# Optimization experiments

Hardware: AMD Instinct MI355X
Metric: run time of the kernel (lower is better)

The kernel has to match this reference:

```python
import jax, jax.numpy as jnp
import numpy as np

DIM = 768
NUM_HEADS = 12
HEAD_DIM = DIM // NUM_HEADS
SCALE = HEAD_DIM ** -0.5


def setup_inputs() -> dict:
    key = jax.random.key(0)
    k_x, k_qkv, k_proj, k_pb = jax.random.split(key, 4)
    B, N = 16, 1024
    x = jax.random.normal(k_x, (B, N, DIM), dtype=jnp.float32)
    # nn.Linear weights: stored as [out, in]; qkv_bias=False -> no qkv bias
    w_qkv = jax.random.normal(k_qkv, (3 * DIM, DIM), dtype=jnp.float32) * (DIM ** -0.5)
    w_proj = jax.random.normal(k_proj, (DIM, DIM), dtype=jnp.float32) * (DIM ** -0.5)
    b_proj = jax.random.normal(k_pb, (DIM,), dtype=jnp.float32) * 0.01
    return {"x": x, "w_qkv": w_qkv, "w_proj": w_proj, "b_proj": b_proj}


def reference(x, w_qkv, w_proj, b_proj):
    B, N, C = x.shape
    H, D = NUM_HEADS, HEAD_DIM
    # qkv projection: [B,N,3C] -> [3,B,H,N,D]
    qkv = jnp.einsum('bnc,oc->bno', x, w_qkv)
    qkv = qkv.reshape(B, N, 3, H, D).transpose(2, 0, 3, 1, 4)
    q, k, v = qkv[0], qkv[1], qkv[2]
    # scaled dot-product attention (dropout ratios are 0.0 -> identity)
    attn = jnp.einsum('bhnd,bhmd->bhnm', q, k) * SCALE
    attn = jax.nn.softmax(attn, axis=-1)
    out = jnp.einsum('bhnm,bhmd->bhnd', attn, v)
    out = out.transpose(0, 2, 1, 3).reshape(B, N, C)
    # output projection
    return jnp.einsum('bnc,oc->bno', out, w_proj) + b_proj
```

## Files before the change

### kernel.cpp

```cpp
#include <hip/hip_runtime.h>
#include <hip/hip_bf16.h>
#include <stdint.h>

typedef unsigned short u16;
typedef unsigned int   u32;
typedef short bf16x8 __attribute__((ext_vector_type(8)));
typedef float f32x4  __attribute__((ext_vector_type(4)));
typedef float f32x16 __attribute__((ext_vector_type(16)));

#define MFMA16(A,B,C) __builtin_amdgcn_mfma_f32_16x16x32_bf16((A),(B),(C),0,0,0)
#define MFMA32(A,B,C) __builtin_amdgcn_mfma_f32_32x32x16_bf16((A),(B),(C),0,0,0)

__device__ __forceinline__ u16 f2b(float x) {
  u32 u = __float_as_uint(x);
  u += 0x7fffu + ((u >> 16) & 1u);
  return (u16)(u >> 16);
}
__device__ __forceinline__ u32 cvtpk(float lo, float hi) {
  u32 r;
  asm("v_cvt_pk_bf16_f32 %0, %1, %2" : "=v"(r) : "v"(lo), "v"(hi));
  return r;
}

typedef __attribute__((address_space(1))) const void glob_void;
typedef __attribute__((address_space(3))) void lds_void;
__device__ __forceinline__ void gld16(const void* g, void* s) {
  __builtin_amdgcn_global_load_lds((glob_void*)g, (lds_void*)s, 16, 0, 0);
}

__global__ void cvt_bf16(const float4* __restrict__ in, ushort4* __restrict__ out, int n4) {
  int stride = gridDim.x * blockDim.x;
  for (int i = blockIdx.x * blockDim.x + threadIdx.x; i < n4; i += stride) {
    float4 v = in[i];
    ushort4 o;
    o.x = f2b(v.x); o.y = f2b(v.y); o.z = f2b(v.z); o.w = f2b(v.w);
    out[i] = o;
  }
}

__global__ __launch_bounds__(256) void gemm_qkv(
    const u16* __restrict__ xb, const u16* __restrict__ wb,
    u16* __restrict__ q, u16* __restrict__ k, u16* __restrict__ vt)
{
  __shared__ u16 lA[2][128*32];
  __shared__ u16 lB[2][128*32];
  const int tid = threadIdx.x;
  const int lane = tid & 63;
  const int wv = tid >> 6;
  const int wr = wv >> 1, wc = wv & 1;
  const int m0 = blockIdx.x << 7;
  const int o0 = blockIdx.y << 7;
  f32x4 acc[4][4] = {};
  const int srow = tid >> 2;
  const int sb   = (((tid & 3) ^ ((srow >> 1) & 3)) << 4);
  const char* gA0 = (const char*)(xb + (size_t)(m0 + srow)      * 768) + sb;
  const char* gA1 = (const char*)(xb + (size_t)(m0 + 64 + srow) * 768) + sb;
  const char* gB0 = (const char*)(wb + (size_t)(o0 + srow)      * 768) + sb;
  const char* gB1 = (const char*)(wb + (size_t)(o0 + 64 + srow) * 768) + sb;
  char* sA = (char*)lA + tid * 16;
  char* sB = (char*)lB + tid * 16;
  const int frow = lane & 15;
  const int fk   = (((lane >> 4) ^ ((frow >> 1) & 3)) << 4);

#define QKV_STAGE(buf, kt) do { const int kb_ = (kt) << 6; const int bo_ = (buf) << 13; \
    gld16(gA0 + kb_, sA + bo_); gld16(gA1 + kb_, sA + bo_ + 4096); \
    gld16(gB0 + kb_, sB + bo_); gld16(gB1 + kb_, sB + bo_ + 4096); } while (0)

  QKV_STAGE(0, 0);
  asm volatile("s_waitcnt vmcnt(0) lgkmcnt(0)" ::: "memory");
  __builtin_amdgcn_s_barrier();
  for (int kt = 0; kt < 24; ++kt) {
    const int cur = kt & 1;
    if (kt < 23) QKV_STAGE(cur ^ 1, kt + 1);
    const char* bA = (const char*)lA + (cur << 13);
    const char* bB = (const char*)lB + (cur << 13);
    bf16x8 af[4], bfr[4];
#pragma unroll
    for (int m = 0; m < 4; ++m)
      af[m] = *(const bf16x8*)(bA + ((wr*64 + m*16 + frow) << 6) + fk);
#pragma unroll
    for (int n = 0; n < 4; ++n)
      bfr[n] = *(const bf16x8*)(bB + ((wc*64 + n*16 + frow) << 6) + fk);
#pragma unroll
    for (int m = 0; m < 4; ++m)
#pragma unroll
      for (int n = 0; n < 4; ++n)
        acc[m][n] = MFMA16(af[m], bfr[n], acc[m][n]);
    asm volatile("s_waitcnt vmcnt(0) lgkmcnt(0)" ::: "memory");
    __builtin_amdgcn_s_barrier();
  }
  const int which = o0 / 768;
  const int ob = o0 - which * 768;
  const float QSCALE = 0.18033688011112042f;
#pragma unroll
  for (int n = 0; n < 4; ++n) {
    const int go = ob + wc*64 + n*16 + (lane & 15);
    const int h = go >> 6, d = go & 63;
#pragma unroll
    for (int m = 0; m < 4; ++m) {
      const int gm0 = m0 + wr*64 + m*16 + ((lane >> 4) << 2);
      const int b = gm0 >> 10, nn0 = gm0 & 1023;
      if (which == 2) {
        ushort4 o4;
        o4.x = f2b(acc[m][n][0]); o4.y = f2b(acc[m][n][1]);
        o4.z = f2b(acc[m][n][2]); o4.w = f2b(acc[m][n][3]);
        *(ushort4*)(vt + (((size_t)((b*12 + h)*64 + d)) << 10) + nn0) = o4;
      } else if (which == 0) {
#pragma unroll
        for (int r = 0; r < 4; ++r)
          q[((size_t)((b*12 + h)*1024 + nn0 + r) << 6) + d] = f2b(acc[m][n][r] * QSCALE);
      } else {
#pragma unroll
        for (int r = 0; r < 4; ++r)
          k[((size_t)((b*12 + h)*1024 + nn0 + r) << 6) + d] = f2b(acc[m][n][r]);
      }
    }
  }
}

__global__ __launch_bounds__(256) void attn_fwd(
    const u16* __restrict__ q, const u16* __restrict__ kk,
    const u16* __restrict__ vt, u16* __restrict__ ao)
{
  __shared__ u16 lK[2][64*64];
  __shared__ u16 lV[2][64*64];
  const int tid = threadIdx.x, lane = tid & 63, wv = tid >> 6;
  const int l31 = lane & 31, hh = lane >> 5;
  const int bh = blockIdx.x, qt = blockIdx.y;
  const u16*  qb = q  + ((size_t)bh << 16);
  const char* kg = (const char*)(kk + ((size_t)bh << 16));
  const char* vg = (const char*)(vt + ((size_t)bh << 16));
  const int qrow = (qt << 7) + (wv << 5) + l31;
  bf16x8 qreg[4];
#pragma unroll
  for (int c = 0; c < 4; ++c)
    qreg[c] = *(const bf16x8*)((const char*)qb + (size_t)qrow*128 + c*32 + hh*16);
  f32x16 ot[2] = {};
  float mrun = -1e30f, lrun = 0.f;
  const int o1 = tid << 4, o2 = o1 + 4096;
  const int ko1 = o1 ^ (((o1 >> 7) & 7) << 4);
  const int ko2 = o2 ^ (((o2 >> 7) & 7) << 4);
  const int d1 = o1 >> 7, d2 = o2 >> 7;
  const int vo1 = d1*2048 + ((o1 & 127) ^ ((d1 & 7) << 4));
  const int vo2 = d2*2048 + ((o2 & 127) ^ ((d2 & 7) << 4));
  char* sK = (char*)lK;
  char* sV = (char*)lV;

#define ATTN_STAGE(buf, t) do { const int bo_ = (buf) << 13; \
    gld16(kg + ((t) << 13) + ko1, sK + bo_ + o1); \
    gld16(kg + ((t) << 13) + ko2, sK + bo_ + o2); \
    gld16(vg + ((t) << 7) + vo1, sV + bo_ + o1); \
    gld16(vg + ((t) << 7) + vo2, sV + bo_ + o2); } while (0)

  ATTN_STAGE(0, 0);
  asm volatile("s_waitcnt vmcnt(0) lgkmcnt(0)" ::: "memory");
  __builtin_amdgcn_s_barrier();
  for (int t0 = 0; t0 < 16; ++t0) {
    const int cur = t0 & 1;
    if (t0 < 15) ATTN_STAGE(cur ^ 1, t0 + 1);
    const char* bK = (const char*)lK + (cur << 13);
    const char* bV = (const char*)lV + (cur << 13);
    f32x16 s[2] = {};
#pragma unroll
    for (int tt = 0; tt < 2; ++tt) {
      const int row = (tt << 5) + l31;
      const int rb = row << 7;
      const int sw = (row & 7) << 4;
#pragma unroll
      for (int c = 0; c < 4; ++c) {
        bf16x8 kf = *(const bf16x8*)(bK + rb + (((c << 5) + (hh << 4)) ^ sw));
        s[tt] = MFMA32(kf, qreg[c], s[tt]);
      }
    }
    float mloc = s[0][0];
#pragma unroll
    for (int tt = 0; tt < 2; ++tt)
#pragma unroll
      for (int r = 0; r < 16; ++r) mloc = fmaxf(mloc, s[tt][r]);
    if (!__all(mloc <= mrun + 8.f)) {
      mloc = fmaxf(mloc, __shfl_xor(mloc, 32));
      const float mnew  = fmaxf(mrun, mloc);
      const float alpha = __builtin_amdgcn_exp2f(mrun - mnew);
      lrun *= alpha;
#pragma unroll
      for (int dt = 0; dt < 2; ++dt)
#pragma unroll
        for (int r = 0; r < 16; ++r) ot[dt][r] *= alpha;
      mrun = mnew;
    }
    float sum = 0.f;
#pragma unroll
    for (int tt = 0; tt < 2; ++tt)
#pragma unroll
      for (int r = 0; r < 16; ++r) {
        s[tt][r] = __builtin_amdgcn_exp2f(s[tt][r] - mrun);
        sum += s[tt][r];
      }
    sum += __shfl_xor(sum, 32);
    lrun += sum;
    bf16x8 pb[4];
#pragma unroll
    for (int tt = 0; tt < 2; ++tt) {
      u32 x0 = cvtpk(s[tt][0],  s[tt][1]);
      u32 y0 = cvtpk(s[tt][4],  s[tt][5]);
      u32 x1 = cvtpk(s[tt][2],  s[tt][3]);
      u32 y1 = cvtpk(s[tt][6],  s[tt][7]);
      asm("v_permlane32_swap_b32 %0, %1" : "+v"(x0), "+v"(y0));
      asm("v_permlane32_swap_b32 %0, %1" : "+v"(x1), "+v"(y1));
      u32 x2 = cvtpk(s[tt][8],  s[tt][9]);
      u32 y2 = cvtpk(s[tt][12], s[tt][13]);
      u32 x3 = cvtpk(s[tt][10], s[tt][11]);
      u32 y3 = cvtpk(s[tt][14], s[tt][15]);
      asm("v_permlane32_swap_b32 %0, %1" : "+v"(x2), "+v"(y2));
      asm("v_permlane32_swap_b32 %0, %1" : "+v"(x3), "+v"(y3));
      union { u32 u[4]; bf16x8 v; } a, b;
      a.u[0] = x0; a.u[1] = x1; a.u[2] = y0; a.u[3] = y1;
      b.u[0] = x2; b.u[1] = x3; b.u[2] = y2; b.u[3] = y3;
      pb[2*tt]     = a.v;
      pb[2*tt + 1] = b.v;
    }
#pragma unroll
    for (int dt = 0; dt < 2; ++dt) {
      const int row = (dt << 5) + l31;
      const int rb = row << 7;
      const int sw = (row & 7) << 4;
#pragma unroll
      for (int cc = 0; cc < 4; ++cc) {
        bf16x8 vf = *(const bf16x8*)(bV + rb + (((cc << 5) + (hh << 4)) ^ sw));
        ot[dt] = MFMA32(vf, pb[cc], ot[dt]);
      }
    }
    asm volatile("s_waitcnt vmcnt(0) lgkmcnt(0)" ::: "memory");
    __builtin_amdgcn_s_barrier();
  }
  const float linv = 1.f / lrun;
  const int b = bh / 12, h = bh - b * 12;
  u16* po = ao + ((size_t)(b*1024 + qrow)) * 768 + h*64;
#pragma unroll
  for (int dt = 0; dt < 2; ++dt) {
#pragma unroll
    for (int g = 0; g < 4; ++g) {
      ushort4 o4;
      o4.x = f2b(ot[dt][4*g + 0] * linv);
      o4.y = f2b(ot[dt][4*g + 1] * linv);
      o4.z = f2b(ot[dt][4*g + 2] * linv);
      o4.w = f2b(ot[dt][4*g + 3] * linv);
      *(ushort4*)(po + dt*32 + g*8 + hh*4) = o4;
    }
  }
}

__global__ __launch_bounds__(256) void gemm_proj(
    const u16* __restrict__ ab, const u16* __restrict__ wb,
    const float* __restrict__ bias, float* __restrict__ out)
{
  __shared__ u16 lA[2][128*32];
  __shared__ u16 lB[2][128*32];
  const int tid = threadIdx.x;
  const int lane = tid & 63;
  const int wv = tid >> 6;
  const int wr = wv >> 1, wc = wv & 1;
  const int m0 = blockIdx.x << 7;
  const int o0 = blockIdx.y << 7;
  f32x4 acc[4][4] = {};
  const int srow = tid >> 2;
  const int sb   = (((tid & 3) ^ ((srow >> 1) & 3)) << 4);
  const char* gA0 = (const char*)(ab + (size_t)(m0 + srow)      * 768) + sb;
  const char* gA1 = (const char*)(ab + (size_t)(m0 + 64 + srow) * 768) + sb;
  const char* gB0 = (const char*)(wb + (size_t)(o0 + srow)      * 768) + sb;
  const char* gB1 = (const char*)(wb + (size_t)(o0 + 64 + srow) * 768) + sb;
  char* sA = (char*)lA + tid * 16;
  char* sB = (char*)lB + tid * 16;
  const int frow = lane & 15;
  const int fk   = (((lane >> 4) ^ ((frow >> 1) & 3)) << 4);

  QKV_STAGE(0, 0);
  asm volatile("s_waitcnt vmcnt(0) lgkmcnt(0)" ::: "memory");
  __builtin_amdgcn_s_barrier();
  for (int kt = 0; kt < 24; ++kt) {
    const int cur = kt & 1;
    if (kt < 23) QKV_STAGE(cur ^ 1, kt + 1);
    const char* bA = (const char*)lA + (cur << 13);
    const char* bB = (const char*)lB + (cur << 13);
    bf16x8 af[4], bfr[4];
#pragma unroll
    for (int m = 0; m < 4; ++m)
      af[m] = *(const bf16x8*)(bA + ((wr*64 + m*16 + frow) << 6) + fk);
#pragma unroll
    for (int n = 0; n < 4; ++n)
      bfr[n] = *(const bf16x8*)(bB + ((wc*64 + n*16 + frow) << 6) + fk);
#pragma unroll
    for (int m = 0; m < 4; ++m)
#pragma unroll
      for (int n = 0; n < 4; ++n)
        acc[m][n] = MFMA16(af[m], bfr[n], acc[m][n]);
    asm volatile("s_waitcnt vmcnt(0) lgkmcnt(0)" ::: "memory");
    __builtin_amdgcn_s_barrier();
  }
#pragma unroll
  for (int n = 0; n < 4; ++n) {
    const int go = o0 + wc*64 + n*16 + (lane & 15);
    const float bv = bias[go];
#pragma unroll
    for (int m = 0; m < 4; ++m) {
#pragma unroll
      for (int r = 0; r < 4; ++r) {
        const int gm = m0 + wr*64 + m*16 + ((lane >> 4) << 2) + r;
        out[(size_t)gm * 768 + go] = acc[m][n][r] + bv;
      }
    }
  }
}

extern "C" void kernel_launch(void* const* d_in, const int* in_sizes, int n_in,
                              void* d_out, int out_size, void* d_ws, size_t ws_size,
                              hipStream_t stream)
{
  (void)in_sizes; (void)n_in; (void)out_size; (void)ws_size;
  const float* x  = (const float*)d_in[0];
  const float* wq = (const float*)d_in[1];
  const float* wp = (const float*)d_in[2];
  const float* bp = (const float*)d_in[3];
  float* out = (float*)d_out;
  char* ws = (char*)d_ws;
  u16* xb     = (u16*)(ws);
  u16* wqkvb  = (u16*)(ws + 25165824);
  u16* wprojb = (u16*)(ws + 28704768);
  u16* qa     = (u16*)(ws + 29884416);
  u16* ka     = (u16*)(ws + 55050240);
  u16* vta    = (u16*)(ws + 80216064);
  u16* ao     = xb;

  cvt_bf16<<<2048, 256, 0, stream>>>((const float4*)x,  (ushort4*)xb,     3145728);
  cvt_bf16<<<1024, 256, 0, stream>>>((const float4*)wq, (ushort4*)wqkvb,   442368);
  cvt_bf16<<< 576, 256, 0, stream>>>((const float4*)wp, (ushort4*)wprojb,  147456);
  gemm_qkv<<<dim3(128, 18), 256, 0, stream>>>(xb, wqkvb, qa, ka, vta);
  attn_fwd<<<dim3(192, 8), 256, 0, stream>>>(qa, ka, vta, ao);
  gemm_proj<<<dim3(128, 6), 256, 0, stream>>>(ao, wprojb, bp, out);
}
```

Measured before the change: 215.9 us.

## Compute softmax row sums via MFMA with ones matrix and raise MFMA priority

The attention kernel stops summing exponentials with VALU adds and a cross-lane shuffle. It instead accumulates the row sum by multiplying the bf16 probabilities against a ones matrix with four extra MFMAs per tile. The row max now uses a tree reduction, and LDS offsets are precomputed outside the loop. s_setprio is raised around the MFMA blocks to favour matrix issue across waves. This trades VALU and shuffle work for more matrix-core work, and the sum now uses bf16-rounded probabilities, which keeps it consistent with the PV product.

```diff
diff --git a/kernel.cpp b/kernel.cpp
--- a/kernel.cpp
+++ b/kernel.cpp
@@ -135,8 +135,11 @@
 #pragma unroll
   for (int c = 0; c < 4; ++c)
     qreg[c] = *(const bf16x8*)((const char*)qb + (size_t)qrow*128 + c*32 + hh*16);
+  const short ONE = (short)0x3f80;
+  const bf16x8 ones = {ONE, ONE, ONE, ONE, ONE, ONE, ONE, ONE};
   f32x16 ot[2] = {};
-  float mrun = -1e30f, lrun = 0.f;
+  f32x16 accl = {};
+  float mrun = -1e30f;
   const int o1 = tid << 4, o2 = o1 + 4096;
   const int ko1 = o1 ^ (((o1 >> 7) & 7) << 4);
   const int ko2 = o2 ^ (((o2 >> 7) & 7) << 4);
@@ -145,6 +148,13 @@
   const int vo2 = d2*2048 + ((o2 & 127) ^ ((d2 & 7) << 4));
   char* sK = (char*)lK;
   char* sV = (char*)lV;
+  const int sw   = (l31 & 7) << 4;
+  const int off0 = ((0 << 5) + (hh << 4)) ^ sw;
+  const int off1 = ((1 << 5) + (hh << 4)) ^ sw;
+  const int off2 = ((2 << 5) + (hh << 4)) ^ sw;
+  const int off3 = ((3 << 5) + (hh << 4)) ^ sw;
+  const int rb0  = l31 << 7;
+  const int rb1  = (32 + l31) << 7;
 
 #define ATTN_STAGE(buf, t) do { const int bo_ = (buf) << 13; \
     gld16(kg + ((t) << 13) + ko1, sK + bo_ + o1); \
@@ -161,43 +171,39 @@
     const char* bK = (const char*)lK + (cur << 13);
     const char* bV = (const char*)lV + (cur << 13);
     f32x16 s[2] = {};
+    __builtin_amdgcn_s_setprio(1);
 #pragma unroll
     for (int tt = 0; tt < 2; ++tt) {
-      const int row = (tt << 5) + l31;
-      const int rb = row << 7;
-      const int sw = (row & 7) << 4;
-#pragma unroll
-      for (int c = 0; c < 4; ++c) {
-        bf16x8 kf = *(const bf16x8*)(bK + rb + (((c << 5) + (hh << 4)) ^ sw));
-        s[tt] = MFMA32(kf, qreg[c], s[tt]);
-      }
-    }
-    float mloc = s[0][0];
-#pragma unroll
-    for (int tt = 0; tt < 2; ++tt)
-#pragma unroll
-      for (int r = 0; r < 16; ++r) mloc = fmaxf(mloc, s[tt][r]);
+      const char* kr = bK + (tt ? rb1 : rb0);
+      s[tt] = MFMA32(*(const bf16x8*)(kr + off0), qreg[0], s[tt]);
+      s[tt] = MFMA32(*(const bf16x8*)(kr + off1), qreg[1], s[tt]);
+      s[tt] = MFMA32(*(const bf16x8*)(kr + off2), qreg[2], s[tt]);
+      s[tt] = MFMA32(*(const bf16x8*)(kr + off3), qreg[3], s[tt]);
+    }
+    __builtin_amdgcn_s_setprio(0);
+    float t8[8];
+#pragma unroll
+    for (int r = 0; r < 8; ++r)
+      t8[r] = fmaxf(fmaxf(s[0][r], s[0][r+8]), fmaxf(s[1][r], s[1][r+8]));
+    const float ta = fmaxf(fmaxf(t8[0], t8[1]), fmaxf(t8[2], t8[3]));
+    const float tb = fmaxf(fmaxf(t8[4], t8[5]), fmaxf(t8[6], t8[7]));
+    float mloc = fmaxf(ta, tb);
     if (!__all(mloc <= mrun + 8.f)) {
       mloc = fmaxf(mloc, __shfl_xor(mloc, 32));
       const float mnew  = fmaxf(mrun, mloc);
       const float alpha = __builtin_amdgcn_exp2f(mrun - mnew);
-      lrun *= alpha;
+      accl[0] *= alpha;
 #pragma unroll
       for (int dt = 0; dt < 2; ++dt)
 #pragma unroll
         for (int r = 0; r < 16; ++r) ot[dt][r] *= alpha;
       mrun = mnew;
     }
-    float sum = 0.f;
 #pragma unroll
     for (int tt = 0; tt < 2; ++tt)
 #pragma unroll
-      for (int r = 0; r < 16; ++r) {
+      for (int r = 0; r < 16; ++r)
         s[tt][r] = __builtin_amdgcn_exp2f(s[tt][r] - mrun);
-        sum += s[tt][r];
-      }
-    sum += __shfl_xor(sum, 32);
-    lrun += sum;
     bf16x8 pb[4];
 #pragma unroll
     for (int tt = 0; tt < 2; ++tt) {
@@ -219,21 +225,24 @@
       pb[2*tt]     = a.v;
       pb[2*tt + 1] = b.v;
     }
+    __builtin_amdgcn_s_setprio(1);
+    accl = MFMA32(ones, pb[0], accl);
+    accl = MFMA32(ones, pb[1], accl);
+    accl = MFMA32(ones, pb[2], accl);
+    accl = MFMA32(ones, pb[3], accl);
 #pragma unroll
     for (int dt = 0; dt < 2; ++dt) {
-      const int row = (dt << 5) + l31;
-      const int rb = row << 7;
-      const int sw = (row & 7) << 4;
-#pragma unroll
-      for (int cc = 0; cc < 4; ++cc) {
-        bf16x8 vf = *(const bf16x8*)(bV + rb + (((cc << 5) + (hh << 4)) ^ sw));
-        ot[dt] = MFMA32(vf, pb[cc], ot[dt]);
-      }
-    }
+      const char* vr = bV + (dt ? rb1 : rb0);
+      ot[dt] = MFMA32(*(const bf16x8*)(vr + off0), pb[0], ot[dt]);
+      ot[dt] = MFMA32(*(const bf16x8*)(vr + off1), pb[1], ot[dt]);
+      ot[dt] = MFMA32(*(const bf16x8*)(vr + off2), pb[2], ot[dt]);
+      ot[dt] = MFMA32(*(const bf16x8*)(vr + off3), pb[3], ot[dt]);
+    }
+    __builtin_amdgcn_s_setprio(0);
     asm volatile("s_waitcnt vmcnt(0) lgkmcnt(0)" ::: "memory");
     __builtin_amdgcn_s_barrier();
   }
-  const float linv = 1.f / lrun;
+  const float linv = 1.f / accl[0];
   const int b = bh / 12, h = bh - b * 12;
   u16* po = ao + ((size_t)(b*1024 + qrow)) * 768 + h*64;
 #pragma unroll
```

Result: no change. 219.0 us (+1.4%).
